# Performance work log

Hardware: AMD Instinct MI355X
Metric: run time of the kernel (lower is better)

The kernel has to match this reference:

```python
import jax, jax.numpy as jnp
import numpy as np

N_USER = 100_000
N_ITEM = 100_000
E = 1_600_000
D_IN = 64
D_OUT = 64


def setup_inputs() -> dict:
    key = jax.random.key(0)
    ks = jax.random.split(key, 14)
    inp = {
        "feat_user": jax.random.normal(ks[0], (N_USER, D_IN), jnp.float32),
        "feat_item": jax.random.normal(ks[1], (N_ITEM, D_IN), jnp.float32),
        "W_follows": jax.random.normal(ks[2], (D_OUT, D_IN), jnp.float32) * 0.05,
        "b_follows": jax.random.normal(ks[3], (D_OUT,), jnp.float32) * 0.05,
        "W_rates": jax.random.normal(ks[4], (D_OUT, D_IN), jnp.float32) * 0.05,
        "b_rates": jax.random.normal(ks[5], (D_OUT,), jnp.float32) * 0.05,
        "W_ratedby": jax.random.normal(ks[6], (D_OUT, D_IN), jnp.float32) * 0.05,
        "b_ratedby": jax.random.normal(ks[7], (D_OUT,), jnp.float32) * 0.05,
        "src_follows": jax.random.randint(ks[8], (E,), 0, N_USER, jnp.int32),
        "dst_follows": jax.random.randint(ks[9], (E,), 0, N_USER, jnp.int32),
        "src_rates": jax.random.randint(ks[10], (E,), 0, N_USER, jnp.int32),
        "dst_rates": jax.random.randint(ks[11], (E,), 0, N_ITEM, jnp.int32),
        "src_ratedby": jax.random.randint(ks[12], (E,), 0, N_ITEM, jnp.int32),
        "dst_ratedby": jax.random.randint(ks[13], (E,), 0, N_USER, jnp.int32),
    }
    return inp


def _mean_agg(Wh, src, dst, num_dst):
    # copy_u + mean: gather projected src features per edge, segment-mean into dst nodes.
    msg_sum = jax.ops.segment_sum(Wh[src], dst, num_segments=num_dst)  # [num_dst, D_OUT]
    cnt = jax.ops.segment_sum(jnp.ones(src.shape, Wh.dtype), dst, num_segments=num_dst)
    return msg_sum / jnp.maximum(cnt, 1.0)[:, None]  # zero-in-degree nodes -> 0 (DGL behavior)


def reference(feat_user, feat_item, W_follows, b_follows, W_rates, b_rates,
              W_ratedby, b_ratedby, src_follows, dst_follows, src_rates,
              dst_rates, src_ratedby, dst_ratedby):
    # Per-etype linear projection on source node features (nn.Linear: x @ W.T + b)
    Wh_f = feat_user @ W_follows.T + b_follows    # user -follows-> user
    Wh_r = feat_user @ W_rates.T + b_rates        # user -rates-> item
    Wh_rb = feat_item @ W_ratedby.T + b_ratedby   # item -rated_by-> user
    # Per-etype mean aggregation, then 'sum' cross-reducer per destination ntype
    h_user = (_mean_agg(Wh_f, src_follows, dst_follows, N_USER)
              + _mean_agg(Wh_rb, src_ratedby, dst_ratedby, N_USER))
    h_item = _mean_agg(Wh_r, src_rates, dst_rates, N_ITEM)
    return jnp.stack([h_user, h_item])  # [2, 100000, 64]
```

## Files before the change

### kernel.cpp

```cpp
#include <hip/hip_runtime.h>

#define D 64
#define NPB_SHIFT 9
#define NPB (1 << NPB_SHIFT)
#define NB 196
#define CHUNK 8192

typedef float f32x4 __attribute__((ext_vector_type(4)));
typedef short bf16x8 __attribute__((ext_vector_type(8)));

__device__ __forceinline__ unsigned bf16rne(float x) {
    unsigned u = __float_as_uint(x);
    return (u + 0x7fffu + ((u >> 16) & 1u)) >> 16;
}

__global__ __launch_bounds__(256) void to_bf16(
    const float* __restrict__ fu, const float* __restrict__ fi,
    unsigned* __restrict__ bu, unsigned* __restrict__ bi, int n4)
{
    const float4* src = blockIdx.y == 0 ? (const float4*)fu : (const float4*)fi;
    uint2* dst = blockIdx.y == 0 ? (uint2*)bu : (uint2*)bi;
    for (int i = blockIdx.x * 256 + threadIdx.x; i < n4; i += gridDim.x * 256) {
        const float4 v = src[i];
        uint2 r;
        r.x = bf16rne(v.x) | (bf16rne(v.y) << 16);
        r.y = bf16rne(v.z) | (bf16rne(v.w) << 16);
        dst[i] = r;
    }
}

__global__ __launch_bounds__(256) void wcvt(
    const float* __restrict__ w0, const float* __restrict__ w1,
    const float* __restrict__ w2, unsigned* __restrict__ dst)
{
    const float* w = blockIdx.x == 0 ? w0 : (blockIdx.x == 1 ? w1 : w2);
    unsigned* o = dst + blockIdx.x * 2048;
    for (int i = threadIdx.x; i < 2048; i += 256)
        o[i] = bf16rne(w[2 * i]) | (bf16rne(w[2 * i + 1]) << 16);
}

__global__ __launch_bounds__(256) void bkt_hist(
    const int* __restrict__ d0, const int* __restrict__ d1, const int* __restrict__ d2,
    int* __restrict__ hist, int nE)
{
    const int et = blockIdx.y;
    const int* dst = et == 0 ? d0 : (et == 1 ? d1 : d2);
    __shared__ int h[NB];
    for (int i = threadIdx.x; i < NB; i += 256) h[i] = 0;
    __syncthreads();
    for (int e = blockIdx.x * 256 + threadIdx.x; e < nE; e += gridDim.x * 256)
        atomicAdd(&h[dst[e] >> NPB_SHIFT], 1);
    __syncthreads();
    int* gh = hist + et * NB;
    for (int i = threadIdx.x; i < NB; i += 256)
        if (h[i]) atomicAdd(&gh[i], h[i]);
}

__global__ __launch_bounds__(256) void bkt_scan(
    const int* __restrict__ hist, int* __restrict__ off, int* __restrict__ gcur)
{
    const int et = blockIdx.x;
    const int tid = threadIdx.x;
    const int v = tid < NB ? hist[et * NB + tid] : 0;
    int inc = v;
#pragma unroll
    for (int of = 1; of < 64; of <<= 1) {
        int t = __shfl_up(inc, of);
        if ((tid & 63) >= of) inc += t;
    }
    __shared__ int ws[4];
    if ((tid & 63) == 63) ws[tid >> 6] = inc;
    __syncthreads();
    int woff = 0;
    for (int i = 0; i < (tid >> 6); ++i) woff += ws[i];
    const int excl = woff + inc - v;
    if (tid < NB) { off[et * NB + tid] = excl; gcur[et * NB + tid] = excl; }
}

__global__ __launch_bounds__(256) void bkt_multisplit(
    const int* __restrict__ s0, const int* __restrict__ d0,
    const int* __restrict__ s1, const int* __restrict__ d1,
    const int* __restrict__ s2, const int* __restrict__ d2,
    int* __restrict__ gcur, int* __restrict__ bkt, int nE, int E)
{
    const int et = blockIdx.y;
    const int* src = et == 0 ? s0 : (et == 1 ? s1 : s2);
    const int* dst = et == 0 ? d0 : (et == 1 ? d1 : d2);
    int* gc = gcur + et * NB;
    int* bk = bkt + (size_t)et * E;

    __shared__ int h[NB];
    __shared__ int st[NB];
    __shared__ int cu[NB];
    __shared__ int gb[NB];
    __shared__ int ws[4];
    __shared__ int stage[CHUNK];

    const int tid = threadIdx.x;
    const int e0 = blockIdx.x * CHUNK;
    const int e1 = min(e0 + CHUNK, nE);

    for (int i = tid; i < NB; i += 256) h[i] = 0;
    __syncthreads();
    for (int e = e0 + tid; e < e1; e += 256)
        atomicAdd(&h[dst[e] >> NPB_SHIFT], 1);
    __syncthreads();

    const int v = tid < NB ? h[tid] : 0;
    int inc = v;
#pragma unroll
    for (int of = 1; of < 64; of <<= 1) {
        int t = __shfl_up(inc, of);
        if ((tid & 63) >= of) inc += t;
    }
    if ((tid & 63) == 63) ws[tid >> 6] = inc;
    __syncthreads();
    int woff = 0;
    for (int i = 0; i < (tid >> 6); ++i) woff += ws[i];
    const int excl = woff + inc - v;
    if (tid < NB) {
        st[tid] = excl;
        cu[tid] = excl;
        if (v > 0) gb[tid] = atomicAdd(&gc[tid], v);
    }
    __syncthreads();

    for (int e = e0 + tid; e < e1; e += 256) {
        const int dd = dst[e];
        const int b = dd >> NPB_SHIFT;
        const int pos = atomicAdd(&cu[b], 1);
        stage[pos] = src[e] | ((dd & (NPB - 1)) << 17);
    }
    __syncthreads();

    const int wv = tid >> 6, ln = tid & 63;
    for (int b = wv; b < NB; b += 4) {
        const int cb = h[b];
        if (cb == 0) continue;
        const int base = st[b], g = gb[b];
        for (int i = ln; i < cb; i += 64)
            bk[g + i] = stage[base + i];
    }
}

__global__ __launch_bounds__(256) void bkt_csr(
    const int* __restrict__ off, const int* __restrict__ bkt_all,
    int* __restrict__ rp_all, int* __restrict__ cnt_all, int* __restrict__ lst_all,
    int N, int E)
{
    const int et = blockIdx.y;
    const int b = blockIdx.x;
    const int* o = off + et * NB;
    const int* bk = bkt_all + (size_t)et * E;
    int* lst = lst_all + (size_t)et * E;
    int* rp  = rp_all  + (size_t)et * N;
    int* cnt = cnt_all + (size_t)et * N;
    const int A  = o[b];
    const int Bb = (b + 1 < NB) ? o[b + 1] : E;

    __shared__ int h[NPB];
    __shared__ int cu[NPB];
    __shared__ int ws2[4];
    for (int i = threadIdx.x; i < NPB; i += 256) h[i] = 0;
    __syncthreads();
    for (int i = A + threadIdx.x; i < Bb; i += 256)
        atomicAdd(&h[((unsigned)bk[i]) >> 17], 1);
    __syncthreads();

    const int tid = threadIdx.x;
    const int v0 = h[2 * tid], v1 = h[2 * tid + 1];
    const int tsum = v0 + v1;
    int inc = tsum;
#pragma unroll
    for (int of = 1; of < 64; of <<= 1) {
        int t = __shfl_up(inc, of);
        if ((tid & 63) >= of) inc += t;
    }
    if ((tid & 63) == 63) ws2[tid >> 6] = inc;
    __syncthreads();
    int woff = 0;
    for (int i = 0; i < (tid >> 6); ++i) woff += ws2[i];
    const int excl = woff + inc - tsum;
    cu[2 * tid] = excl;
    cu[2 * tid + 1] = excl + v0;
    const int n0 = b << NPB_SHIFT;
    if (n0 + 2 * tid < N)     { cnt[n0 + 2 * tid]     = v0; rp[n0 + 2 * tid]     = A + excl; }
    if (n0 + 2 * tid + 1 < N) { cnt[n0 + 2 * tid + 1] = v1; rp[n0 + 2 * tid + 1] = A + excl + v0; }
    __syncthreads();

    for (int i = A + threadIdx.x; i < Bb; i += 256) {
        const int w = bk[i];
        const int dl = ((unsigned)w) >> 17;
        const int pos = atomicAdd(&cu[dl], 1);
        lst[A + pos] = w & 0x1FFFF;
    }
}

template <bool RMW>
__global__ __launch_bounds__(256) void gather_proj_mfma(
    const unsigned* __restrict__ feat,
    const int* __restrict__ rp, const int* __restrict__ cnt, const int* __restrict__ lst,
    const uint4* __restrict__ Wb,
    const float* __restrict__ bias,
    float* __restrict__ out, int N)
{
    __shared__ unsigned meanL[16][36];
    __shared__ int degL[16];

    const int tid = threadIdx.x;
    const int wv = tid >> 6;
    const int l  = tid & 63;
    const int k  = l & 31;
    const int p  = l >> 5;
    const int bbase = blockIdx.x * 16;

#pragma unroll 1
    for (int q = 0; q < 4; ++q) {
        const int nl = wv * 4 + q;
        const int n = bbase + nl;
        const int deg = (n < N) ? cnt[n] : 0;
        float sx = 0.0f, sy = 0.0f;
        if (deg > 0) {
            const int start = rp[n];
            int id[8];
            float mk[8];
#pragma unroll
            for (int j = 0; j < 8; ++j) {
                const int ee = 2 * j + p;
                id[j] = lst[start + (ee < deg ? ee : deg - 1)];
                mk[j] = ee < deg ? 1.0f : 0.0f;
            }
            for (int e = 0; e < deg; e += 16) {
                unsigned w[8];
#pragma unroll
                for (int j = 0; j < 8; ++j)
                    w[j] = feat[id[j] * 32 + k];
                const bool more = (e + 16) < deg;
                int id2[8];
                float mk2[8];
                if (more) {
#pragma unroll
                    for (int j = 0; j < 8; ++j) {
                        const int ee = e + 16 + 2 * j + p;
                        id2[j] = lst[start + (ee < deg ? ee : deg - 1)];
                        mk2[j] = ee < deg ? 1.0f : 0.0f;
                    }
                }
#pragma unroll
                for (int j = 0; j < 8; ++j) {
                    sx = fmaf(mk[j], __uint_as_float(w[j] << 16), sx);
                    sy = fmaf(mk[j], __uint_as_float(w[j] & 0xffff0000u), sy);
                }
                if (more) {
#pragma unroll
                    for (int j = 0; j < 8; ++j) { id[j] = id2[j]; mk[j] = mk2[j]; }
                }
            }
        }
        sx += __shfl_xor(sx, 32);
        sy += __shfl_xor(sy, 32);
        const float inv = deg > 0 ? 1.0f / (float)deg : 0.0f;
        if (p == 0)
            meanL[nl][k] = bf16rne(sx * inv) | (bf16rne(sy * inv) << 16);
        if (l == 0) degL[nl] = deg;
    }
    __syncthreads();

    const int m16 = l & 15;
    const int qq  = l >> 4;
    union { uint4 u; bf16x8 v; } b0, b1, a0, a1;
    b0.u = Wb[(wv * 16 + m16) * 8 + qq];
    b1.u = Wb[(wv * 16 + m16) * 8 + qq + 4];
    a0.u = *reinterpret_cast<const uint4*>(&meanL[m16][qq * 4]);
    a1.u = *reinterpret_cast<const uint4*>(&meanL[m16][16 + qq * 4]);

    f32x4 d = {0.0f, 0.0f, 0.0f, 0.0f};
    d = __builtin_amdgcn_mfma_f32_16x16x32_bf16(a0.v, b0.v, d, 0, 0, 0);
    d = __builtin_amdgcn_mfma_f32_16x16x32_bf16(a1.v, b1.v, d, 0, 0, 0);

    const int o = wv * 16 + m16;
    const float bo = bias[o];
#pragma unroll
    for (int r = 0; r < 4; ++r) {
        const int nl = qq * 4 + r;
        const int gn = bbase + nl;
        if (gn < N) {
            float res = d[r] + (degL[nl] > 0 ? bo : 0.0f);
            if (RMW) res += out[(size_t)gn * D + o];
            out[(size_t)gn * D + o] = res;
        }
    }
}

extern "C" void kernel_launch(void* const* d_in, const int* in_sizes, int n_in,
                              void* d_out, int out_size, void* d_ws, size_t ws_size,
                              hipStream_t stream)
{
    const float* feat_user = (const float*)d_in[0];
    const float* feat_item = (const float*)d_in[1];
    const float* W_f  = (const float*)d_in[2];
    const float* b_f  = (const float*)d_in[3];
    const float* W_r  = (const float*)d_in[4];
    const float* b_r  = (const float*)d_in[5];
    const float* W_rb = (const float*)d_in[6];
    const float* b_rb = (const float*)d_in[7];
    const int* src_f  = (const int*)d_in[8];
    const int* dst_f  = (const int*)d_in[9];
    const int* src_r  = (const int*)d_in[10];
    const int* dst_r  = (const int*)d_in[11];
    const int* src_rb = (const int*)d_in[12];
    const int* dst_rb = (const int*)d_in[13];
    float* out = (float*)d_out;

    const int NU = in_sizes[0] / D;
    const int NI = in_sizes[1] / D;
    const int E  = in_sizes[8];
    const int N  = NU;

    int* hist = (int*)d_ws;
    int* off  = hist + 3 * NB;
    int* gcur = off  + 3 * NB;
    int* rp   = gcur + 3 * NB;
    int* cnt  = rp   + 3 * (size_t)N;
    int* bkt  = cnt  + 3 * (size_t)N;
    int* lst  = bkt  + 3 * (size_t)E;
    unsigned* Wbf = (unsigned*)(lst + 3 * (size_t)E);
    unsigned* fbu = Wbf + 3 * 2048;
    unsigned* fbi = fbu + (size_t)N * 32;

    hipMemsetAsync(hist, 0, (size_t)3 * NB * sizeof(int), stream);

    const dim3 blk(256);
    const int n4 = N * D / 4;
    to_bf16<<<dim3(2048, 2), blk, 0, stream>>>(feat_user, feat_item, fbu, fbi, n4);
    wcvt<<<3, blk, 0, stream>>>(W_f, W_rb, W_r, Wbf);

    bkt_hist<<<dim3(256, 3), blk, 0, stream>>>(dst_f, dst_rb, dst_r, hist, E);
    bkt_scan<<<3, blk, 0, stream>>>(hist, off, gcur);
    const int nms = (E + CHUNK - 1) / CHUNK;
    bkt_multisplit<<<dim3(nms, 3), blk, 0, stream>>>(
        src_f, dst_f, src_rb, dst_rb, src_r, dst_r, gcur, bkt, E, E);
    bkt_csr<<<dim3(NB, 3), blk, 0, stream>>>(off, bkt, rp, cnt, lst, N, E);

    int* rp_f  = rp;            int* cnt_f  = cnt;            int* lst_f  = lst;
    int* rp_rb = rp + N;        int* cnt_rb = cnt + N;        int* lst_rb = lst + E;
    int* rp_r  = rp + 2 * N;    int* cnt_r  = cnt + 2 * N;    int* lst_r  = lst + 2 * (size_t)E;

    const int gblk = (N + 15) / 16;
    gather_proj_mfma<false><<<gblk, blk, 0, stream>>>(
        fbu, rp_f, cnt_f, lst_f, (const uint4*)Wbf, b_f, out, NU);
    gather_proj_mfma<true><<<gblk, blk, 0, stream>>>(
        fbi, rp_rb, cnt_rb, lst_rb, (const uint4*)(Wbf + 2048), b_rb, out, NU);
    gather_proj_mfma<false><<<gblk, blk, 0, stream>>>(
        fbu, rp_r, cnt_r, lst_r, (const uint4*)(Wbf + 4096), b_r,
        out + (size_t)NU * D, NI);
}
```

Measured before the change: 303.6 us.

## Fuse user-side etype gathers into one kernel and merge prep launches

Combines the bf16 feature conversion, weight conversion and bucket histogram into a single prep launch with a 2D grid partitioned by role. The two user-destination aggregations (follows and rated_by) now run in one kernel that keeps both means in shared memory and accumulates both projections into one MFMA result. This removes the read-modify-write pass over the user half of the output and two kernel launches. The cost is more shared memory and registers per block in the fused gather kernel.

```diff
diff --git a/kernel.cpp b/kernel.cpp
--- a/kernel.cpp
+++ b/kernel.cpp
@@ -5,6 +5,7 @@
 #define NPB (1 << NPB_SHIFT)
 #define NB 196
 #define CHUNK 8192
+#define HB 256
 
 typedef float f32x4 __attribute__((ext_vector_type(4)));
 typedef short bf16x8 __attribute__((ext_vector_type(8)));
@@ -14,46 +15,51 @@
     return (u + 0x7fffu + ((u >> 16) & 1u)) >> 16;
 }
 
-__global__ __launch_bounds__(256) void to_bf16(
+__global__ __launch_bounds__(256) void prep(
     const float* __restrict__ fu, const float* __restrict__ fi,
-    unsigned* __restrict__ bu, unsigned* __restrict__ bi, int n4)
-{
-    const float4* src = blockIdx.y == 0 ? (const float4*)fu : (const float4*)fi;
-    uint2* dst = blockIdx.y == 0 ? (uint2*)bu : (uint2*)bi;
-    for (int i = blockIdx.x * 256 + threadIdx.x; i < n4; i += gridDim.x * 256) {
-        const float4 v = src[i];
-        uint2 r;
-        r.x = bf16rne(v.x) | (bf16rne(v.y) << 16);
-        r.y = bf16rne(v.z) | (bf16rne(v.w) << 16);
-        dst[i] = r;
-    }
-}
-
-__global__ __launch_bounds__(256) void wcvt(
+    unsigned* __restrict__ bu, unsigned* __restrict__ bi, int n4,
     const float* __restrict__ w0, const float* __restrict__ w1,
-    const float* __restrict__ w2, unsigned* __restrict__ dst)
-{
-    const float* w = blockIdx.x == 0 ? w0 : (blockIdx.x == 1 ? w1 : w2);
-    unsigned* o = dst + blockIdx.x * 2048;
-    for (int i = threadIdx.x; i < 2048; i += 256)
-        o[i] = bf16rne(w[2 * i]) | (bf16rne(w[2 * i + 1]) << 16);
-}
-
-__global__ __launch_bounds__(256) void bkt_hist(
+    const float* __restrict__ w2, unsigned* __restrict__ wdst,
     const int* __restrict__ d0, const int* __restrict__ d1, const int* __restrict__ d2,
     int* __restrict__ hist, int nE)
 {
-    const int et = blockIdx.y;
-    const int* dst = et == 0 ? d0 : (et == 1 ? d1 : d2);
-    __shared__ int h[NB];
-    for (int i = threadIdx.x; i < NB; i += 256) h[i] = 0;
-    __syncthreads();
-    for (int e = blockIdx.x * 256 + threadIdx.x; e < nE; e += gridDim.x * 256)
-        atomicAdd(&h[dst[e] >> NPB_SHIFT], 1);
-    __syncthreads();
-    int* gh = hist + et * NB;
-    for (int i = threadIdx.x; i < NB; i += 256)
-        if (h[i]) atomicAdd(&gh[i], h[i]);
+    const int y = blockIdx.y;
+    const int bx = blockIdx.x;
+    const int tid = threadIdx.x;
+    if (y < 2) {
+        const float4* src = y == 0 ? (const float4*)fu : (const float4*)fi;
+        uint2* dst = y == 0 ? (uint2*)bu : (uint2*)bi;
+        for (int i = bx * 256 + tid; i < n4; i += 2048 * 256) {
+            const float4 v = src[i];
+            uint2 r;
+            r.x = bf16rne(v.x) | (bf16rne(v.y) << 16);
+            r.y = bf16rne(v.z) | (bf16rne(v.w) << 16);
+            dst[i] = r;
+        }
+        return;
+    }
+    if (bx == 0) {
+        for (int i = tid; i < 3 * 2048; i += 256) {
+            const int et = i >> 11, idx = i & 2047;
+            const float* w = et == 0 ? w0 : (et == 1 ? w1 : w2);
+            wdst[i] = bf16rne(w[2 * idx]) | (bf16rne(w[2 * idx + 1]) << 16);
+        }
+        return;
+    }
+    if (bx <= 3 * HB) {
+        const int et = (bx - 1) / HB;
+        const int b2 = (bx - 1) % HB;
+        const int* dst = et == 0 ? d0 : (et == 1 ? d1 : d2);
+        __shared__ int h[NB];
+        for (int i = tid; i < NB; i += 256) h[i] = 0;
+        __syncthreads();
+        for (int e = b2 * 256 + tid; e < nE; e += HB * 256)
+            atomicAdd(&h[dst[e] >> NPB_SHIFT], 1);
+        __syncthreads();
+        int* gh = hist + et * NB;
+        for (int i = tid; i < NB; i += 256)
+            if (h[i]) atomicAdd(&gh[i], h[i]);
+    }
 }
 
 __global__ __launch_bounds__(256) void bkt_scan(
@@ -196,16 +202,64 @@
     }
 }
 
-template <bool RMW>
-__global__ __launch_bounds__(256) void gather_proj_mfma(
-    const unsigned* __restrict__ feat,
-    const int* __restrict__ rp, const int* __restrict__ cnt, const int* __restrict__ lst,
-    const uint4* __restrict__ Wb,
-    const float* __restrict__ bias,
+__device__ __forceinline__ void gather_mean(
+    const unsigned* __restrict__ feat, const int* __restrict__ lst,
+    int start, int deg, int k, int p, float& mx, float& my)
+{
+    float sx = 0.0f, sy = 0.0f;
+    if (deg > 0) {
+        int id[8];
+        float mk[8];
+#pragma unroll
+        for (int j = 0; j < 8; ++j) {
+            const int ee = 2 * j + p;
+            id[j] = lst[start + (ee < deg ? ee : deg - 1)];
+            mk[j] = ee < deg ? 1.0f : 0.0f;
+        }
+        for (int e = 0; e < deg; e += 16) {
+            unsigned w[8];
+#pragma unroll
+            for (int j = 0; j < 8; ++j)
+                w[j] = feat[id[j] * 32 + k];
+            const bool more = (e + 16) < deg;
+            int id2[8];
+            float mk2[8];
+            if (more) {
+#pragma unroll
+                for (int j = 0; j < 8; ++j) {
+                    const int ee = e + 16 + 2 * j + p;
+                    id2[j] = lst[start + (ee < deg ? ee : deg - 1)];
+                    mk2[j] = ee < deg ? 1.0f : 0.0f;
+                }
+            }
+#pragma unroll
+            for (int j = 0; j < 8; ++j) {
+                sx = fmaf(mk[j], __uint_as_float(w[j] << 16), sx);
+                sy = fmaf(mk[j], __uint_as_float(w[j] & 0xffff0000u), sy);
+            }
+            if (more) {
+#pragma unroll
+                for (int j = 0; j < 8; ++j) { id[j] = id2[j]; mk[j] = mk2[j]; }
+            }
+        }
+    }
+    sx += __shfl_xor(sx, 32);
+    sy += __shfl_xor(sy, 32);
+    const float inv = deg > 0 ? 1.0f / (float)deg : 0.0f;
+    mx = sx * inv;
+    my = sy * inv;
+}
+
+__global__ __launch_bounds__(256) void gather_user2(
+    const unsigned* __restrict__ fbu, const unsigned* __restrict__ fbi,
+    const int* __restrict__ rpF, const int* __restrict__ cntF, const int* __restrict__ lstF,
+    const int* __restrict__ rpR, const int* __restrict__ cntR, const int* __restrict__ lstR,
+    const uint4* __restrict__ WbF, const uint4* __restrict__ WbR,
+    const float* __restrict__ bF, const float* __restrict__ bR,
     float* __restrict__ out, int N)
 {
-    __shared__ unsigned meanL[16][36];
-    __shared__ int degL[16];
+    __shared__ unsigned meanL[2][16][36];
+    __shared__ int degL[2][16];
 
     const int tid = threadIdx.x;
     const int wv = tid >> 6;
@@ -215,53 +269,86 @@
     const int bbase = blockIdx.x * 16;
 
 #pragma unroll 1
+    for (int et = 0; et < 2; ++et) {
+        const unsigned* feat = et ? fbi : fbu;
+        const int* rp  = et ? rpR  : rpF;
+        const int* cnt = et ? cntR : cntF;
+        const int* lst = et ? lstR : lstF;
+#pragma unroll 1
+        for (int q = 0; q < 4; ++q) {
+            const int nl = wv * 4 + q;
+            const int n = bbase + nl;
+            const int deg = (n < N) ? cnt[n] : 0;
+            const int start = deg > 0 ? rp[n] : 0;
+            float mx, my;
+            gather_mean(feat, lst, start, deg, k, p, mx, my);
+            if (p == 0)
+                meanL[et][nl][k] = bf16rne(mx) | (bf16rne(my) << 16);
+            if (l == 0) degL[et][nl] = deg;
+        }
+    }
+    __syncthreads();
+
+    const int m16 = l & 15;
+    const int qq  = l >> 4;
+    union { uint4 u; bf16x8 v; } bf0, bf1, br0, br1, a;
+    bf0.u = WbF[(wv * 16 + m16) * 8 + qq];
+    bf1.u = WbF[(wv * 16 + m16) * 8 + qq + 4];
+    br0.u = WbR[(wv * 16 + m16) * 8 + qq];
+    br1.u = WbR[(wv * 16 + m16) * 8 + qq + 4];
+
+    f32x4 d = {0.0f, 0.0f, 0.0f, 0.0f};
+    a.u = *reinterpret_cast<const uint4*>(&meanL[0][m16][qq * 4]);
+    d = __builtin_amdgcn_mfma_f32_16x16x32_bf16(a.v, bf0.v, d, 0, 0, 0);
+    a.u = *reinterpret_cast<const uint4*>(&meanL[0][m16][16 + qq * 4]);
+    d = __builtin_amdgcn_mfma_f32_16x16x32_bf16(a.v, bf1.v, d, 0, 0, 0);
+    a.u = *reinterpret_cast<const uint4*>(&meanL[1][m16][qq * 4]);
+    d = __builtin_amdgcn_mfma_f32_16x16x32_bf16(a.v, br0.v, d, 0, 0, 0);
+    a.u = *reinterpret_cast<const uint4*>(&meanL[1][m16][16 + qq * 4]);
+    d = __builtin_amdgcn_mfma_f32_16x16x32_bf16(a.v, br1.v, d, 0, 0, 0);
+
+    const int o = wv * 16 + m16;
+    const float boF = bF[o];
+    const float boR = bR[o];
+#pragma unroll
+    for (int r = 0; r < 4; ++r) {
+        const int nl = qq * 4 + r;
+        const int gn = bbase + nl;
+        if (gn < N) {
+            float res = d[r];
+            if (degL[0][nl] > 0) res += boF;
+            if (degL[1][nl] > 0) res += boR;
+            out[(size_t)gn * D + o] = res;
+        }
+    }
+}
+
+__global__ __launch_bounds__(256) void gather_proj_mfma(
+    const unsigned* __restrict__ feat,
+    const int* __restrict__ rp, const int* __restrict__ cnt, const int* __restrict__ lst,
+    const uint4* __restrict__ Wb, const float* __restrict__ bias,
+    float* __restrict__ out, int N)
+{
+    __shared__ unsigned meanL[16][36];
+    __shared__ int degL[16];
+
+    const int tid = threadIdx.x;
+    const int wv = tid >> 6;
+    const int l  = tid & 63;
+    const int k  = l & 31;
+    const int p  = l >> 5;
+    const int bbase = blockIdx.x * 16;
+
+#pragma unroll 1
     for (int q = 0; q < 4; ++q) {
         const int nl = wv * 4 + q;
         const int n = bbase + nl;
         const int deg = (n < N) ? cnt[n] : 0;
-        float sx = 0.0f, sy = 0.0f;
-        if (deg > 0) {
-            const int start = rp[n];
-            int id[8];
-            float mk[8];
-#pragma unroll
-            for (int j = 0; j < 8; ++j) {
-                const int ee = 2 * j + p;
-                id[j] = lst[start + (ee < deg ? ee : deg - 1)];
-                mk[j] = ee < deg ? 1.0f : 0.0f;
-            }
-            for (int e = 0; e < deg; e += 16) {
-                unsigned w[8];
-#pragma unroll
-                for (int j = 0; j < 8; ++j)
-                    w[j] = feat[id[j] * 32 + k];
-                const bool more = (e + 16) < deg;
-                int id2[8];
-                float mk2[8];
-                if (more) {
-#pragma unroll
-                    for (int j = 0; j < 8; ++j) {
-                        const int ee = e + 16 + 2 * j + p;
-                        id2[j] = lst[start + (ee < deg ? ee : deg - 1)];
-                        mk2[j] = ee < deg ? 1.0f : 0.0f;
-                    }
-                }
-#pragma unroll
-                for (int j = 0; j < 8; ++j) {
-                    sx = fmaf(mk[j], __uint_as_float(w[j] << 16), sx);
-                    sy = fmaf(mk[j], __uint_as_float(w[j] & 0xffff0000u), sy);
-                }
-                if (more) {
-#pragma unroll
-                    for (int j = 0; j < 8; ++j) { id[j] = id2[j]; mk[j] = mk2[j]; }
-                }
-            }
-        }
-        sx += __shfl_xor(sx, 32);
-        sy += __shfl_xor(sy, 32);
-        const float inv = deg > 0 ? 1.0f / (float)deg : 0.0f;
+        const int start = deg > 0 ? rp[n] : 0;
+        float mx, my;
+        gather_mean(feat, lst, start, deg, k, p, mx, my);
         if (p == 0)
-            meanL[nl][k] = bf16rne(sx * inv) | (bf16rne(sy * inv) << 16);
+            meanL[nl][k] = bf16rne(mx) | (bf16rne(my) << 16);
         if (l == 0) degL[nl] = deg;
     }
     __syncthreads();
@@ -286,7 +373,6 @@
         const int gn = bbase + nl;
         if (gn < N) {
             float res = d[r] + (degL[nl] > 0 ? bo : 0.0f);
-            if (RMW) res += out[(size_t)gn * D + o];
             out[(size_t)gn * D + o] = res;
         }
     }
@@ -332,10 +418,10 @@
 
     const dim3 blk(256);
     const int n4 = N * D / 4;
-    to_bf16<<<dim3(2048, 2), blk, 0, stream>>>(feat_user, feat_item, fbu, fbi, n4);
-    wcvt<<<3, blk, 0, stream>>>(W_f, W_rb, W_r, Wbf);
-
-    bkt_hist<<<dim3(256, 3), blk, 0, stream>>>(dst_f, dst_rb, dst_r, hist, E);
+    prep<<<dim3(2048, 3), blk, 0, stream>>>(
+        feat_user, feat_item, fbu, fbi, n4,
+        W_f, W_rb, W_r, Wbf,
+        dst_f, dst_rb, dst_r, hist, E);
     bkt_scan<<<3, blk, 0, stream>>>(hist, off, gcur);
     const int nms = (E + CHUNK - 1) / CHUNK;
     bkt_multisplit<<<dim3(nms, 3), blk, 0, stream>>>(
@@ -347,11 +433,10 @@
     int* rp_r  = rp + 2 * N;    int* cnt_r  = cnt + 2 * N;    int* lst_r  = lst + 2 * (size_t)E;
 
     const int gblk = (N + 15) / 16;
-    gather_proj_mfma<false><<<gblk, blk, 0, stream>>>(
-        fbu, rp_f, cnt_f, lst_f, (const uint4*)Wbf, b_f, out, NU);
-    gather_proj_mfma<true><<<gblk, blk, 0, stream>>>(
-        fbi, rp_rb, cnt_rb, lst_rb, (const uint4*)(Wbf + 2048), b_rb, out, NU);
-    gather_proj_mfma<false><<<gblk, blk, 0, stream>>>(
+    gather_user2<<<gblk, blk, 0, stream>>>(
+        fbu, fbi, rp_f, cnt_f, lst_f, rp_rb, cnt_rb, lst_rb,
+        (const uint4*)Wbf, (const uint4*)(Wbf + 2048), b_f, b_rb, out, NU);
+    gather_proj_mfma<<<gblk, blk, 0, stream>>>(
         fbu, rp_r, cnt_r, lst_r, (const uint4*)(Wbf + 4096), b_r,
         out + (size_t)NU * D, NI);
 }
```

Measured after the change: 301.8 us. No clear change (-0.6%).
